# Kernel optimization log

Hardware: AMD Instinct MI355X
Metric: run time of the kernel (lower is better)

Reference implementation:

```python
import jax, jax.numpy as jnp
import numpy as np

# Dimensions
B_, L_, D_ = 2, 1024, 1024
EXPAND, N_STATE, K_CONV = 2, 16, 4
D_INNER = D_ * EXPAND          # 2048
DT_RANK = (D_ + 15) // 16      # 64 (mamba default: ceil(d_model/16))


def setup_inputs() -> dict:
    key = jax.random.key(0)
    ks = jax.random.split(key, 10)
    sc = 0.02
    x = jax.random.normal(ks[0], (B_, L_, D_), jnp.float32)
    ln_w = jnp.ones((D_,), jnp.float32)
    ln_b = jnp.zeros((D_,), jnp.float32)
    W_in = jax.random.normal(ks[1], (2 * D_INNER, D_), jnp.float32) * sc
    W_conv = jax.random.normal(ks[2], (D_INNER, K_CONV), jnp.float32) * 0.2
    b_conv = jnp.zeros((D_INNER,), jnp.float32)
    W_xproj = jax.random.normal(ks[3], (DT_RANK + 2 * N_STATE, D_INNER), jnp.float32) * sc
    W_dt = jax.random.normal(ks[4], (D_INNER, DT_RANK), jnp.float32) * (DT_RANK ** -0.5)
    # dt bias: inverse softplus of dt ~ U[1e-3, 1e-1] (mamba init)
    dt = jnp.exp(jax.random.uniform(ks[5], (D_INNER,), jnp.float32)
                 * (np.log(0.1) - np.log(0.001)) + np.log(0.001))
    b_dt = dt + jnp.log(-jnp.expm1(-dt))
    # A_log init: log(1..N) per channel (S4D-real init)
    A_log = jnp.log(jnp.broadcast_to(jnp.arange(1, N_STATE + 1, dtype=jnp.float32),
                                     (D_INNER, N_STATE)))
    D_skip = jnp.ones((D_INNER,), jnp.float32)
    W_out = jax.random.normal(ks[6], (D_, D_INNER), jnp.float32) * sc
    return {"x": x, "ln_w": ln_w, "ln_b": ln_b, "W_in": W_in, "W_conv": W_conv,
            "b_conv": b_conv, "W_xproj": W_xproj, "W_dt": W_dt, "b_dt": b_dt,
            "A_log": A_log, "D_skip": D_skip, "W_out": W_out}


def _layernorm(x, w, b, eps=1e-5):
    mu = jnp.mean(x, axis=-1, keepdims=True)
    var = jnp.mean(jnp.square(x - mu), axis=-1, keepdims=True)
    return (x - mu) * jax.lax.rsqrt(var + eps) * w + b


def reference(x, ln_w, ln_b, W_in, W_conv, b_conv, W_xproj, W_dt, b_dt,
              A_log, D_skip, W_out):
    B, L, D = x.shape
    residual = x
    xn = _layernorm(x, ln_w, ln_b)

    # in_proj -> (x_ssm, z), each (B, L, d_inner)
    xz = jnp.einsum('bld,ed->ble', xn, W_in)
    xs, z = jnp.split(xz, 2, axis=-1)

    # causal depthwise conv1d along L + SiLU
    xp = jnp.pad(xs, ((0, 0), (K_CONV - 1, 0), (0, 0)))
    xc = b_conv + sum(xp[:, k:k + L, :] * W_conv[:, k] for k in range(K_CONV))
    xc = jax.nn.silu(xc)

    # input-dependent dt, B, C
    dbl = jnp.einsum('ble,re->blr', xc, W_xproj)
    dt_low = dbl[..., :DT_RANK]
    B_ssm = dbl[..., DT_RANK:DT_RANK + N_STATE]        # (B, L, N)
    C_ssm = dbl[..., DT_RANK + N_STATE:]               # (B, L, N)
    delta = jax.nn.softplus(jnp.einsum('blr,er->ble', dt_low, W_dt) + b_dt)  # (B, L, d_inner)

    A = -jnp.exp(A_log)                                # (d_inner, N)
    dA = jnp.exp(delta[..., None] * A)                 # (B, L, d_inner, N)
    dBx = delta[..., None] * B_ssm[:, :, None, :] * xc[..., None]  # (B, L, d_inner, N)

    def step(h, inp):
        dA_t, dBx_t, C_t = inp
        h = dA_t * h + dBx_t                           # (B, d_inner, N)
        y_t = jnp.einsum('bdn,bn->bd', h, C_t)
        return h, y_t

    h0 = jnp.zeros((B, D_INNER, N_STATE), x.dtype)
    _, ys = jax.lax.scan(step, h0,
                         (dA.transpose(1, 0, 2, 3), dBx.transpose(1, 0, 2, 3),
                          C_ssm.transpose(1, 0, 2)))
    y = ys.transpose(1, 0, 2) + D_skip * xc            # (B, L, d_inner)
    y = y * jax.nn.silu(z)
    out = jnp.einsum('ble,de->bld', y, W_out)
    # dropout is identity in eval mode
    return out + residual
```

## Files before the change

kernel.cpp:

```cpp
#include <hip/hip_runtime.h>
#include <math.h>

#define B_ 2
#define L_ 1024
#define D_ 1024
#define D_INNER 2048
#define DT_RANK 64
#define N_STATE 16
#define NC 64
#define LC 16

typedef __attribute__((ext_vector_type(8))) short bf16x8;
typedef __attribute__((ext_vector_type(4))) float f32x4;

__device__ __forceinline__ unsigned short f2bf(float f) {
  unsigned int u = __float_as_uint(f);
  u += 0x7fffu + ((u >> 16) & 1u);
  return (unsigned short)(u >> 16);
}
__device__ __forceinline__ float bf2f(unsigned short s) {
  return __uint_as_float((unsigned int)s << 16);
}
__device__ __forceinline__ float softplus_f(float v) {
  return (v > 20.0f) ? v : log1pf(__expf(v));
}

#define N4_WIN  1048576
#define N4_WOUT  524288
#define N4_WDT    32768
#define N4_WXP    65536
#define CVT_BLOCKS ((N4_WIN + N4_WOUT + N4_WDT + N4_WXP + 255) / 256)

__global__ __launch_bounds__(256) void prep_kernel(const float* __restrict__ x,
                                                   const float* __restrict__ w,
                                                   const float* __restrict__ b,
                                                   unsigned short* __restrict__ xn_b,
                                                   const float* __restrict__ W_in,
                                                   const float* __restrict__ W_out,
                                                   const float* __restrict__ W_dt,
                                                   const float* __restrict__ W_xp,
                                                   unsigned short* __restrict__ Win_b,
                                                   unsigned short* __restrict__ Wout_b,
                                                   unsigned short* __restrict__ Wdt_b,
                                                   unsigned short* __restrict__ Wxp_b) {
  if (blockIdx.x < 2048) {
    int row = blockIdx.x;
    int tid = threadIdx.x;
    const float* xr = x + (size_t)row * D_;
    float4 v = ((const float4*)xr)[tid];
    float s  = v.x + v.y + v.z + v.w;
    float s2 = v.x*v.x + v.y*v.y + v.z*v.z + v.w*v.w;
    #pragma unroll
    for (int off = 32; off > 0; off >>= 1) {
      s  += __shfl_down(s, off);
      s2 += __shfl_down(s2, off);
    }
    __shared__ float ss[4], ss2[4];
    int wid = tid >> 6, lane = tid & 63;
    if (lane == 0) { ss[wid] = s; ss2[wid] = s2; }
    __syncthreads();
    if (tid == 0) {
      float a  = ss[0] + ss[1] + ss[2] + ss[3];
      float a2 = ss2[0] + ss2[1] + ss2[2] + ss2[3];
      ss[0]  = a  * (1.0f / D_);
      ss2[0] = a2 * (1.0f / D_);
    }
    __syncthreads();
    float mu = ss[0];
    float var = ss2[0] - mu * mu;
    float rstd = rsqrtf(var + 1e-5f);
    float4 wv = ((const float4*)w)[tid];
    float4 bv = ((const float4*)b)[tid];
    ushort4 o;
    o.x = f2bf((v.x - mu) * rstd * wv.x + bv.x);
    o.y = f2bf((v.y - mu) * rstd * wv.y + bv.y);
    o.z = f2bf((v.z - mu) * rstd * wv.z + bv.z);
    o.w = f2bf((v.w - mu) * rstd * wv.w + bv.w);
    ((ushort4*)(xn_b + (size_t)row * D_))[tid] = o;
    return;
  }
  int i = (blockIdx.x - 2048) * 256 + threadIdx.x;
  if (i < N4_WIN) {
    float4 v = ((const float4*)W_in)[i];
    ushort4 o; o.x = f2bf(v.x); o.y = f2bf(v.y); o.z = f2bf(v.z); o.w = f2bf(v.w);
    ((ushort4*)Win_b)[i] = o;
    return;
  }
  i -= N4_WIN;
  if (i < N4_WOUT) {
    float4 v = ((const float4*)W_out)[i];
    ushort4 o; o.x = f2bf(v.x); o.y = f2bf(v.y); o.z = f2bf(v.z); o.w = f2bf(v.w);
    ((ushort4*)Wout_b)[i] = o;
    return;
  }
  i -= N4_WOUT;
  if (i < N4_WDT) {
    float4 v = ((const float4*)W_dt)[i];
    ushort4 o; o.x = f2bf(v.x); o.y = f2bf(v.y); o.z = f2bf(v.z); o.w = f2bf(v.w);
    ((ushort4*)Wdt_b)[i] = o;
    return;
  }
  i -= N4_WDT;
  if (i < N4_WXP) {
    int row = (i * 4) >> 11;
    ushort4 o = make_ushort4(0, 0, 0, 0);
    if (row < 96) {
      float4 v = ((const float4*)W_xp)[i];
      o.x = f2bf(v.x); o.y = f2bf(v.y); o.z = f2bf(v.z); o.w = f2bf(v.w);
    }
    ((ushort4*)Wxp_b)[i] = o;
  }
}

template<int EPI, int BMT>
__global__ __launch_bounds__(256) void gemm_mfma(const unsigned short* __restrict__ A, int lda,
                                                 const unsigned short* __restrict__ B, int ldb,
                                                 float* __restrict__ Cf,
                                                 unsigned short* __restrict__ Cb,
                                                 int ldc, int Nguard, int K,
                                                 const float* __restrict__ ep0,
                                                 size_t zstride = 0) {
  __shared__ unsigned short As[BMT * 64];
  __shared__ unsigned short Bs[128 * 64];
  const int tid = threadIdx.x;
  const int lane = tid & 63;
  const int w = tid >> 6;
  const int wr = w >> 1, wc = w & 1;
  int flat = blockIdx.y * gridDim.x + blockIdx.x;
  int nwg = gridDim.x * gridDim.y;
  int q8 = nwg >> 3;
  int swz = (flat & 7) * q8 + (flat >> 3);
  const int bm = (swz / gridDim.x) * BMT;
  const int bn = (swz % gridDim.x) * 128;
  const int l16 = lane & 15;
  constexpr int MW = BMT / 32;

  int kbeg = 0, kend = K;
  if (EPI == 4) {
    int ks = K >> 4;
    kbeg = blockIdx.z * ks;
    kend = kbeg + ks;
    Cf += (size_t)blockIdx.z * zstride;
  }

  f32x4 acc[MW][4];
  #pragma unroll
  for (int m = 0; m < MW; ++m)
    #pragma unroll
    for (int n = 0; n < 4; ++n) acc[m][n] = (f32x4){0.f, 0.f, 0.f, 0.f};

  for (int k0 = kbeg; k0 < kend; k0 += 64) {
    #pragma unroll
    for (int i = 0; i < BMT / 32; ++i) {
      int p = (i * 256 + tid) * 16;
      int r = p >> 7;
      int s = (p >> 4) & 7;
      int cb = ((s ^ (r & 7)) << 3);
      const unsigned short* ga = A + (size_t)(bm + r) * lda + k0 + cb;
      __builtin_amdgcn_global_load_lds(
          (const __attribute__((address_space(1))) void*)ga,
          (__attribute__((address_space(3))) void*)(As + (p >> 1)), 16, 0, 0);
    }
    #pragma unroll
    for (int i = 0; i < 4; ++i) {
      int p = (i * 256 + tid) * 16;
      int r = p >> 7;
      int s = (p >> 4) & 7;
      int cb = ((s ^ (r & 7)) << 3);
      const unsigned short* gb = B + (size_t)(bn + r) * ldb + k0 + cb;
      __builtin_amdgcn_global_load_lds(
          (const __attribute__((address_space(1))) void*)gb,
          (__attribute__((address_space(3))) void*)(Bs + (p >> 1)), 16, 0, 0);
    }
    __syncthreads();
    #pragma unroll
    for (int ks = 0; ks < 2; ++ks) {
      const int slot = ks * 4 + (lane >> 4);
      bf16x8 af[MW], bfr[4];
      #pragma unroll
      for (int m = 0; m < MW; ++m) {
        int ar = wr * (BMT / 2) + m * 16 + l16;
        af[m] = *(const bf16x8*)(As + ar * 64 + ((slot ^ (ar & 7)) << 3));
      }
      #pragma unroll
      for (int n = 0; n < 4; ++n) {
        int br = wc * 64 + n * 16 + l16;
        bfr[n] = *(const bf16x8*)(Bs + br * 64 + ((slot ^ (br & 7)) << 3));
      }
      #pragma unroll
      for (int m = 0; m < MW; ++m)
        #pragma unroll
        for (int n = 0; n < 4; ++n)
          acc[m][n] = __builtin_amdgcn_mfma_f32_16x16x32_bf16(af[m], bfr[n], acc[m][n], 0, 0, 0);
    }
    __syncthreads();
  }

  const int crow0 = bm + wr * (BMT / 2) + (lane >> 4) * 4;
  const int ccol0 = bn + wc * 64 + l16;
  #pragma unroll
  for (int m = 0; m < MW; ++m) {
    #pragma unroll
    for (int n = 0; n < 4; ++n) {
      int c = ccol0 + n * 16;
      if (c >= Nguard) continue;
      #pragma unroll
      for (int r = 0; r < 4; ++r) {
        int rr = crow0 + m * 16 + r;
        float v = acc[m][n][r];
        if (EPI == 1) {
          Cb[(size_t)rr * ldc + c] = f2bf(v);
        } else if (EPI == 2) {
          Cf[(size_t)rr * ldc + c] = v + ep0[(size_t)rr * ldc + c];
        } else if (EPI == 5) {
          Cb[(size_t)rr * ldc + c] = f2bf(softplus_f(v + ep0[c]));
        } else {
          Cf[(size_t)rr * ldc + c] = v;
        }
      }
    }
  }
}

__global__ __launch_bounds__(256) void reduce_dbl_kernel(const float* __restrict__ part,
                                                         float* __restrict__ dblb,
                                                         unsigned short* __restrict__ dtlow_b) {
  int i = blockIdx.x * 256 + threadIdx.x;
  float4 a = ((const float4*)part)[i];
  #pragma unroll
  for (int s = 1; s < 16; ++s) {
    float4 b = ((const float4*)part)[s * 49152 + i];
    a.x += b.x; a.y += b.y; a.z += b.z; a.w += b.w;
  }
  ((float4*)dblb)[i] = a;
  int flat = i * 4;
  int row = flat / 96;
  int col = flat - row * 96;
  if (col < 64) {
    ushort4 o; o.x = f2bf(a.x); o.y = f2bf(a.y); o.z = f2bf(a.z); o.w = f2bf(a.w);
    *(ushort4*)(dtlow_b + (size_t)row * 64 + col) = o;
  }
}

__global__ __launch_bounds__(256) void conv_silu_kernel(const unsigned short* __restrict__ xz,
                                                        const float* __restrict__ Wc,
                                                        const float* __restrict__ bc,
                                                        unsigned short* __restrict__ xcb) {
  int idx = blockIdx.x * 256 + threadIdx.x;
  int e = idx & (D_INNER - 1);
  int t = (idx >> 11) & (L_ - 1);
  int bt = idx >> 11;
  float acc = bc[e];
  float w0 = Wc[e * 4 + 0], w1 = Wc[e * 4 + 1], w2 = Wc[e * 4 + 2], w3 = Wc[e * 4 + 3];
  const unsigned short* base = xz + (size_t)bt * 4096 + e;
  if (t >= 3) acc = fmaf(bf2f(base[-3 * 4096]), w0, acc);
  if (t >= 2) acc = fmaf(bf2f(base[-2 * 4096]), w1, acc);
  if (t >= 1) acc = fmaf(bf2f(base[-1 * 4096]), w2, acc);
  acc = fmaf(bf2f(base[0]), w3, acc);
  float s = acc / (1.0f + __expf(-acc));
  xcb[idx] = f2bf(s);
}

__global__ __launch_bounds__(256) void scan1_kernel(const unsigned short* __restrict__ delta,
                                                    const unsigned short* __restrict__ xc,
                                                    const float* __restrict__ dbl,
                                                    const float* __restrict__ A_log,
                                                    float* __restrict__ P,
                                                    float* __restrict__ Q) {
  int e = blockIdx.x * 256 + threadIdx.x;
  int b = blockIdx.y, c = blockIdx.z;
  const int t0 = (int)(b * L_ + c * LC);

  __shared__ float sB[LC][N_STATE];
  {
    int step = threadIdx.x >> 4, n = threadIdx.x & 15;
    sB[step][n] = dbl[(size_t)(t0 + step) * 96 + 64 + n];
  }
  __syncthreads();

  float An[N_STATE];
  #pragma unroll
  for (int q = 0; q < 4; ++q) {
    float4 v = *(const float4*)&A_log[(size_t)e * N_STATE + q * 4];
    An[q*4+0] = -__expf(v.x); An[q*4+1] = -__expf(v.y);
    An[q*4+2] = -__expf(v.z); An[q*4+3] = -__expf(v.w);
  }
  float h[N_STATE], p[N_STATE];
  #pragma unroll
  for (int n = 0; n < N_STATE; ++n) { h[n] = 0.f; p[n] = 1.f; }

  const size_t row0 = (size_t)t0 * D_INNER + e;
  float dlt = bf2f(delta[row0]);
  float xcv = bf2f(xc[row0]);

  for (int tt = 0; tt < LC; ++tt) {
    float ndlt = 0.f, nxcv = 0.f;
    if (tt + 1 < LC) {
      ndlt = bf2f(delta[row0 + (size_t)(tt + 1) * D_INNER]);
      nxcv = bf2f(xc[row0 + (size_t)(tt + 1) * D_INNER]);
    }
    float dbx = dlt * xcv;
    #pragma unroll
    for (int n = 0; n < N_STATE; ++n) {
      float da = __expf(dlt * An[n]);
      h[n] = fmaf(da, h[n], dbx * sB[tt][n]);
      p[n] *= da;
    }
    dlt = ndlt; xcv = nxcv;
  }
  size_t o = ((size_t)(c * B_ + b) * N_STATE) * D_INNER + e;
  #pragma unroll
  for (int n = 0; n < N_STATE; ++n) {
    P[o + (size_t)n * D_INNER] = p[n];
    Q[o + (size_t)n * D_INNER] = h[n];
  }
}

__global__ __launch_bounds__(256) void scan2_kernel(const float* __restrict__ P,
                                                    float* __restrict__ Q) {
  int idx = blockIdx.x * 256 + threadIdx.x;
  float H = 0.f;
  #pragma unroll
  for (int c = 0; c < NC; ++c) {
    size_t o = (size_t)c * (B_ * N_STATE * D_INNER) + idx;
    float p = P[o], q = Q[o];
    Q[o] = H;
    H = fmaf(p, H, q);
  }
}

__global__ __launch_bounds__(256) void scan3_kernel(const unsigned short* __restrict__ delta,
                                                    const unsigned short* __restrict__ xc,
                                                    const float* __restrict__ dbl,
                                                    const float* __restrict__ A_log,
                                                    const float* __restrict__ Hinit,
                                                    const unsigned short* __restrict__ xz,
                                                    const float* __restrict__ Dsk,
                                                    unsigned short* __restrict__ y) {
  int e = blockIdx.x * 256 + threadIdx.x;
  int b = blockIdx.y, c = blockIdx.z;
  const int t0 = (int)(b * L_ + c * LC);

  __shared__ float sB[LC][N_STATE];
  __shared__ float sC[LC][N_STATE];
  {
    int step = threadIdx.x >> 4, n = threadIdx.x & 15;
    const float* row = dbl + (size_t)(t0 + step) * 96;
    sB[step][n] = row[64 + n];
    sC[step][n] = row[80 + n];
  }
  __syncthreads();

  float An[N_STATE];
  #pragma unroll
  for (int q = 0; q < 4; ++q) {
    float4 v = *(const float4*)&A_log[(size_t)e * N_STATE + q * 4];
    An[q*4+0] = -__expf(v.x); An[q*4+1] = -__expf(v.y);
    An[q*4+2] = -__expf(v.z); An[q*4+3] = -__expf(v.w);
  }
  float h[N_STATE];
  {
    size_t o = ((size_t)(c * B_ + b) * N_STATE) * D_INNER + e;
    #pragma unroll
    for (int n = 0; n < N_STATE; ++n) h[n] = Hinit[o + (size_t)n * D_INNER];
  }
  float dskip = Dsk[e];
  const size_t row0 = (size_t)t0 * D_INNER + e;
  const size_t zrow0 = (size_t)t0 * 4096 + D_INNER + e;

  float dlt = bf2f(delta[row0]);
  float xcv = bf2f(xc[row0]);
  float zv  = bf2f(xz[zrow0]);

  for (int tt = 0; tt < LC; ++tt) {
    float ndlt = 0.f, nxcv = 0.f, nzv = 0.f;
    if (tt + 1 < LC) {
      ndlt = bf2f(delta[row0 + (size_t)(tt + 1) * D_INNER]);
      nxcv = bf2f(xc[row0 + (size_t)(tt + 1) * D_INNER]);
      nzv  = bf2f(xz[zrow0 + (size_t)(tt + 1) * 4096]);
    }
    float dbx = dlt * xcv;
    float yv = 0.f;
    #pragma unroll
    for (int n = 0; n < N_STATE; ++n) {
      float da = __expf(dlt * An[n]);
      h[n] = fmaf(da, h[n], dbx * sB[tt][n]);
      yv = fmaf(h[n], sC[tt][n], yv);
    }
    float gate = zv / (1.0f + __expf(-zv));
    y[row0 + (size_t)tt * D_INNER] = f2bf((yv + dskip * xcv) * gate);
    dlt = ndlt; xcv = nxcv; zv = nzv;
  }
}

extern "C" void kernel_launch(void* const* d_in, const int* in_sizes, int n_in,
                              void* d_out, int out_size, void* d_ws, size_t ws_size,
                              hipStream_t stream) {
  const float* x       = (const float*)d_in[0];
  const float* ln_w    = (const float*)d_in[1];
  const float* ln_b    = (const float*)d_in[2];
  const float* W_in    = (const float*)d_in[3];
  const float* W_conv  = (const float*)d_in[4];
  const float* b_conv  = (const float*)d_in[5];
  const float* W_xproj = (const float*)d_in[6];
  const float* W_dt    = (const float*)d_in[7];
  const float* b_dt    = (const float*)d_in[8];
  const float* A_log   = (const float*)d_in[9];
  const float* D_skip  = (const float*)d_in[10];
  const float* W_out   = (const float*)d_in[11];
  float* out = (float*)d_out;

  const size_t BL = (size_t)B_ * L_;
  float* dblb = (float*)d_ws;
  float* part = dblb + 196608;
  float* P    = part + 3145728;
  float* Q    = P    + 4194304;
  unsigned short* xn_b    = (unsigned short*)(Q + 4194304);
  unsigned short* Win_b   = xn_b    + 2097152;
  unsigned short* xz_b    = Win_b   + 4194304;
  unsigned short* xc_b    = xz_b    + 8388608;
  unsigned short* Wxp_b   = xc_b    + 4194304;
  unsigned short* y_b     = Wxp_b   + 262144;
  unsigned short* Wout_b  = y_b     + 4194304;
  unsigned short* dtlow_b = Wout_b  + 2097152;
  unsigned short* Wdt_b   = dtlow_b + 131072;
  unsigned short* delta_b = Wdt_b   + 131072;

  prep_kernel<<<2048 + CVT_BLOCKS, 256, 0, stream>>>(
      x, ln_w, ln_b, xn_b, W_in, W_out, W_dt, W_xproj, Win_b, Wout_b, Wdt_b, Wxp_b);
  gemm_mfma<1, 128><<<dim3(32, 16), 256, 0, stream>>>(
      xn_b, D_, Win_b, D_, nullptr, xz_b, 4096, 4096, D_, nullptr, 0);
  conv_silu_kernel<<<(BL * D_INNER) / 256, 256, 0, stream>>>(xz_b, W_conv, b_conv, xc_b);
  gemm_mfma<4, 128><<<dim3(1, 16, 16), 256, 0, stream>>>(
      xc_b, D_INNER, Wxp_b, D_INNER, part, nullptr, 96, 96, D_INNER, nullptr,
      (size_t)2048 * 96);
  reduce_dbl_kernel<<<192, 256, 0, stream>>>(part, dblb, dtlow_b);
  gemm_mfma<5, 128><<<dim3(16, 16), 256, 0, stream>>>(
      dtlow_b, DT_RANK, Wdt_b, DT_RANK, nullptr, delta_b, D_INNER, D_INNER, DT_RANK, b_dt, 0);
  scan1_kernel<<<dim3(D_INNER / 256, B_, NC), 256, 0, stream>>>(delta_b, xc_b, dblb, A_log, P, Q);
  scan2_kernel<<<(B_ * N_STATE * D_INNER) / 256, 256, 0, stream>>>(P, Q);
  scan3_kernel<<<dim3(D_INNER / 256, B_, NC), 256, 0, stream>>>(delta_b, xc_b, dblb, A_log, Q,
                                                                xz_b, D_skip, y_b);
  gemm_mfma<2, 64><<<dim3(8, 32), 256, 0, stream>>>(
      y_b, D_INNER, Wout_b, D_INNER, out, nullptr, D_, D_, D_INNER, x, 0);
}
```

Measured before the change: 256.3 us.

## Replace split-K partial buffers with atomic accumulation and fold dt_low conversion into GEMM

The x_proj split-K GEMM now atomically adds into a zeroed dbl buffer, so the separate reduction kernel and its partial-sum buffer go away. The dt GEMM reads the fp32 dt_low slice straight from dbl and converts it to bf16 in its load loop. The out_proj GEMM is split over K=2 with atomics into an output pre-filled with the residual by the prep kernel. The aim is fewer launches and less intermediate traffic, paid for with atomic contention, nondeterministic summation order, and register-path loads in the dt GEMM in place of direct-to-LDS loads.

```diff
diff --git a/kernel.cpp b/kernel.cpp
--- a/kernel.cpp
+++ b/kernel.cpp
@@ -29,7 +29,10 @@
 #define N4_WOUT  524288
 #define N4_WDT    32768
 #define N4_WXP    65536
-#define CVT_BLOCKS ((N4_WIN + N4_WOUT + N4_WDT + N4_WXP + 255) / 256)
+#define N4_ZERO   49152
+#define N4_CPY   524288
+#define PREP_F4 (N4_WIN + N4_WOUT + N4_WDT + N4_WXP + N4_ZERO + N4_CPY)
+#define PREP_BLOCKS (2048 + (PREP_F4 + 255) / 256)
 
 __global__ __launch_bounds__(256) void prep_kernel(const float* __restrict__ x,
                                                    const float* __restrict__ w,
@@ -42,7 +45,9 @@
                                                    unsigned short* __restrict__ Win_b,
                                                    unsigned short* __restrict__ Wout_b,
                                                    unsigned short* __restrict__ Wdt_b,
-                                                   unsigned short* __restrict__ Wxp_b) {
+                                                   unsigned short* __restrict__ Wxp_b,
+                                                   float* __restrict__ dblb,
+                                                   float* __restrict__ outb) {
   if (blockIdx.x < 2048) {
     int row = blockIdx.x;
     int tid = threadIdx.x;
@@ -109,6 +114,16 @@
       o.x = f2bf(v.x); o.y = f2bf(v.y); o.z = f2bf(v.z); o.w = f2bf(v.w);
     }
     ((ushort4*)Wxp_b)[i] = o;
+    return;
+  }
+  i -= N4_WXP;
+  if (i < N4_ZERO) {
+    ((float4*)dblb)[i] = make_float4(0.f, 0.f, 0.f, 0.f);
+    return;
+  }
+  i -= N4_ZERO;
+  if (i < N4_CPY) {
+    ((float4*)outb)[i] = ((const float4*)x)[i];
   }
 }
 
@@ -119,7 +134,7 @@
                                                  unsigned short* __restrict__ Cb,
                                                  int ldc, int Nguard, int K,
                                                  const float* __restrict__ ep0,
-                                                 size_t zstride = 0) {
+                                                 const float* __restrict__ Af32 = nullptr) {
   __shared__ unsigned short As[BMT * 64];
   __shared__ unsigned short Bs[128 * 64];
   const int tid = threadIdx.x;
@@ -136,11 +151,10 @@
   constexpr int MW = BMT / 32;
 
   int kbeg = 0, kend = K;
-  if (EPI == 4) {
-    int ks = K >> 4;
+  if (EPI == 4 || EPI == 7) {
+    int ks = K / gridDim.z;
     kbeg = blockIdx.z * ks;
     kend = kbeg + ks;
-    Cf += (size_t)blockIdx.z * zstride;
   }
 
   f32x4 acc[MW][4];
@@ -150,16 +164,33 @@
     for (int n = 0; n < 4; ++n) acc[m][n] = (f32x4){0.f, 0.f, 0.f, 0.f};
 
   for (int k0 = kbeg; k0 < kend; k0 += 64) {
-    #pragma unroll
-    for (int i = 0; i < BMT / 32; ++i) {
-      int p = (i * 256 + tid) * 16;
-      int r = p >> 7;
-      int s = (p >> 4) & 7;
-      int cb = ((s ^ (r & 7)) << 3);
-      const unsigned short* ga = A + (size_t)(bm + r) * lda + k0 + cb;
-      __builtin_amdgcn_global_load_lds(
-          (const __attribute__((address_space(1))) void*)ga,
-          (__attribute__((address_space(3))) void*)(As + (p >> 1)), 16, 0, 0);
+    if constexpr (EPI == 5) {
+      #pragma unroll
+      for (int i = 0; i < BMT / 32; ++i) {
+        int p = (i * 256 + tid) * 16;
+        int r = p >> 7;
+        int s = (p >> 4) & 7;
+        int cb = ((s ^ (r & 7)) << 3);
+        const float* ga = Af32 + (size_t)(bm + r) * lda + cb;
+        float4 v0 = *(const float4*)ga;
+        float4 v1 = *(const float4*)(ga + 4);
+        ushort4 u0 = make_ushort4(f2bf(v0.x), f2bf(v0.y), f2bf(v0.z), f2bf(v0.w));
+        ushort4 u1 = make_ushort4(f2bf(v1.x), f2bf(v1.y), f2bf(v1.z), f2bf(v1.w));
+        *(ushort4*)(As + (p >> 1)) = u0;
+        *(ushort4*)(As + (p >> 1) + 4) = u1;
+      }
+    } else {
+      #pragma unroll
+      for (int i = 0; i < BMT / 32; ++i) {
+        int p = (i * 256 + tid) * 16;
+        int r = p >> 7;
+        int s = (p >> 4) & 7;
+        int cb = ((s ^ (r & 7)) << 3);
+        const unsigned short* ga = A + (size_t)(bm + r) * lda + k0 + cb;
+        __builtin_amdgcn_global_load_lds(
+            (const __attribute__((address_space(1))) void*)ga,
+            (__attribute__((address_space(3))) void*)(As + (p >> 1)), 16, 0, 0);
+      }
     }
     #pragma unroll
     for (int i = 0; i < 4; ++i) {
@@ -210,8 +241,8 @@
         float v = acc[m][n][r];
         if (EPI == 1) {
           Cb[(size_t)rr * ldc + c] = f2bf(v);
-        } else if (EPI == 2) {
-          Cf[(size_t)rr * ldc + c] = v + ep0[(size_t)rr * ldc + c];
+        } else if (EPI == 4 || EPI == 7) {
+          atomicAdd(&Cf[(size_t)rr * ldc + c], v);
         } else if (EPI == 5) {
           Cb[(size_t)rr * ldc + c] = f2bf(softplus_f(v + ep0[c]));
         } else {
@@ -219,26 +250,6 @@
         }
       }
     }
-  }
-}
-
-__global__ __launch_bounds__(256) void reduce_dbl_kernel(const float* __restrict__ part,
-                                                         float* __restrict__ dblb,
-                                                         unsigned short* __restrict__ dtlow_b) {
-  int i = blockIdx.x * 256 + threadIdx.x;
-  float4 a = ((const float4*)part)[i];
-  #pragma unroll
-  for (int s = 1; s < 16; ++s) {
-    float4 b = ((const float4*)part)[s * 49152 + i];
-    a.x += b.x; a.y += b.y; a.z += b.z; a.w += b.w;
-  }
-  ((float4*)dblb)[i] = a;
-  int flat = i * 4;
-  int row = flat / 96;
-  int col = flat - row * 96;
-  if (col < 64) {
-    ushort4 o; o.x = f2bf(a.x); o.y = f2bf(a.y); o.z = f2bf(a.z); o.w = f2bf(a.w);
-    *(ushort4*)(dtlow_b + (size_t)row * 64 + col) = o;
   }
 }
 
@@ -412,8 +423,7 @@
 
   const size_t BL = (size_t)B_ * L_;
   float* dblb = (float*)d_ws;
-  float* part = dblb + 196608;
-  float* P    = part + 3145728;
+  float* P    = dblb + 196608;
   float* Q    = P    + 4194304;
   unsigned short* xn_b    = (unsigned short*)(Q + 4194304);
   unsigned short* Win_b   = xn_b    + 2097152;
@@ -422,25 +432,23 @@
   unsigned short* Wxp_b   = xc_b    + 4194304;
   unsigned short* y_b     = Wxp_b   + 262144;
   unsigned short* Wout_b  = y_b     + 4194304;
-  unsigned short* dtlow_b = Wout_b  + 2097152;
-  unsigned short* Wdt_b   = dtlow_b + 131072;
+  unsigned short* Wdt_b   = Wout_b  + 2097152;
   unsigned short* delta_b = Wdt_b   + 131072;
 
-  prep_kernel<<<2048 + CVT_BLOCKS, 256, 0, stream>>>(
-      x, ln_w, ln_b, xn_b, W_in, W_out, W_dt, W_xproj, Win_b, Wout_b, Wdt_b, Wxp_b);
+  prep_kernel<<<PREP_BLOCKS, 256, 0, stream>>>(
+      x, ln_w, ln_b, xn_b, W_in, W_out, W_dt, W_xproj,
+      Win_b, Wout_b, Wdt_b, Wxp_b, dblb, out);
   gemm_mfma<1, 128><<<dim3(32, 16), 256, 0, stream>>>(
-      xn_b, D_, Win_b, D_, nullptr, xz_b, 4096, 4096, D_, nullptr, 0);
+      xn_b, D_, Win_b, D_, nullptr, xz_b, 4096, 4096, D_, nullptr);
   conv_silu_kernel<<<(BL * D_INNER) / 256, 256, 0, stream>>>(xz_b, W_conv, b_conv, xc_b);
   gemm_mfma<4, 128><<<dim3(1, 16, 16), 256, 0, stream>>>(
-      xc_b, D_INNER, Wxp_b, D_INNER, part, nullptr, 96, 96, D_INNER, nullptr,
-      (size_t)2048 * 96);
-  reduce_dbl_kernel<<<192, 256, 0, stream>>>(part, dblb, dtlow_b);
+      xc_b, D_INNER, Wxp_b, D_INNER, dblb, nullptr, 96, 96, D_INNER, nullptr);
   gemm_mfma<5, 128><<<dim3(16, 16), 256, 0, stream>>>(
-      dtlow_b, DT_RANK, Wdt_b, DT_RANK, nullptr, delta_b, D_INNER, D_INNER, DT_RANK, b_dt, 0);
+      nullptr, 96, Wdt_b, DT_RANK, nullptr, delta_b, D_INNER, D_INNER, DT_RANK, b_dt, dblb);
   scan1_kernel<<<dim3(D_INNER / 256, B_, NC), 256, 0, stream>>>(delta_b, xc_b, dblb, A_log, P, Q);
   scan2_kernel<<<(B_ * N_STATE * D_INNER) / 256, 256, 0, stream>>>(P, Q);
   scan3_kernel<<<dim3(D_INNER / 256, B_, NC), 256, 0, stream>>>(delta_b, xc_b, dblb, A_log, Q,
                                                                 xz_b, D_skip, y_b);
-  gemm_mfma<2, 64><<<dim3(8, 32), 256, 0, stream>>>(
-      y_b, D_INNER, Wout_b, D_INNER, out, nullptr, D_, D_, D_INNER, x, 0);
-}
+  gemm_mfma<7, 64><<<dim3(8, 32, 2), 256, 0, stream>>>(
+      y_b, D_INNER, Wout_b, D_INNER, out, nullptr, D_, D_, D_INNER, nullptr);
+}
```

Result: no change. 258.1 us (+0.7%).
